# Performance work log

Hardware: AMD Instinct MI355X
Metric: run time of the kernel (lower is better)

The kernel has to match this reference:

```python
import jax, jax.numpy as jnp
import numpy as np

B, S, D_IN, D_OUT, H = 4, 2048, 1024, 1024, 16
HD = D_OUT // H  # 64


def setup_inputs() -> dict:
    key = jax.random.key(0)
    ks = jax.random.split(key, 6)
    s = 1.0 / np.sqrt(D_IN)
    return {
        "x": jax.random.normal(ks[0], (B, S, D_IN), dtype=jnp.float32),
        "Wq": jax.random.uniform(ks[1], (D_IN, D_OUT), jnp.float32, -s, s),
        "Wk": jax.random.uniform(ks[2], (D_IN, D_OUT), jnp.float32, -s, s),
        "Wv": jax.random.uniform(ks[3], (D_IN, D_OUT), jnp.float32, -s, s),
        "Wo": jax.random.uniform(ks[4], (D_OUT, D_OUT), jnp.float32, -s, s),
        "bo": jax.random.uniform(ks[5], (D_OUT,), jnp.float32, -s, s),
    }


def reference(x, Wq, Wk, Wv, Wo, bo):
    b, s, _ = x.shape
    # QKV projections -> [b, H, s, hd]
    def split_heads(t):
        return t.reshape(b, s, H, HD).transpose(0, 2, 1, 3)
    q = split_heads(x @ Wq)
    k = split_heads(x @ Wk)
    v = split_heads(x @ Wv)
    # attention scores [b, H, s, s]
    scores = jnp.einsum("bhqd,bhkd->bhqk", q, k)
    causal = jnp.triu(jnp.ones((s, s), dtype=bool), k=1)
    scores = jnp.where(causal, -jnp.inf, scores)
    attn = jax.nn.softmax(scores / np.sqrt(HD), axis=-1)
    ctx = jnp.einsum("bhqk,bhkd->bhqd", attn, v)
    ctx = ctx.transpose(0, 2, 1, 3).reshape(b, s, D_OUT)
    return ctx @ Wo + bo
```

## Files before the change

kernel.cpp:

```cpp
#include <hip/hip_runtime.h>

typedef __attribute__((ext_vector_type(8))) short bf16x8;
typedef __attribute__((ext_vector_type(4))) float f32x4;
typedef __attribute__((ext_vector_type(4))) unsigned uint4v;

#define SM_C 0.18033688011112042f
#define SM_M 20.0f
#define MFMA16 __builtin_amdgcn_mfma_f32_16x16x32_bf16

__device__ __forceinline__ unsigned short f2bf(float f) {
  unsigned u = __builtin_bit_cast(unsigned, f);
  u += 0x7fffu + ((u >> 16) & 1u);
  return (unsigned short)(u >> 16);
}

__device__ __forceinline__ unsigned cvtpk(float lo, float hi) {
  unsigned r;
  asm volatile("v_cvt_pk_bf16_f32 %0, %1, %2" : "=v"(r) : "v"(lo), "v"(hi));
  return r;
}

__device__ __forceinline__ void gload16(const void* g, void* lds) {
  __builtin_amdgcn_global_load_lds(
      (const __attribute__((address_space(1))) void*)g,
      (__attribute__((address_space(3))) void*)lds, 16, 0, 0);
}

#define BARRIER __builtin_amdgcn_s_barrier()
#define LGKM0 asm volatile("s_waitcnt lgkmcnt(0)" ::: "memory")

__global__ __launch_bounds__(256) void prep(const float* __restrict__ x,
                                            unsigned short* __restrict__ xb,
                                            const float* __restrict__ W0,
                                            const float* __restrict__ W1,
                                            const float* __restrict__ W2,
                                            const float* __restrict__ W3,
                                            unsigned short* __restrict__ WT) {
  __shared__ float tile[32][33];
  const int bid = blockIdx.x;
  if (bid < 2048) {
    int i = bid * 256 + threadIdx.x;
    for (; i < 2097152; i += 2048 * 256) {
      float4 v = ((const float4*)x)[i];
      unsigned long long packed = (unsigned long long)f2bf(v.x) |
                                  ((unsigned long long)f2bf(v.y) << 16) |
                                  ((unsigned long long)f2bf(v.z) << 32) |
                                  ((unsigned long long)f2bf(v.w) << 48);
      ((unsigned long long*)xb)[i] = packed;
    }
  } else {
    int b2 = bid - 2048;
    const int z = b2 >> 10;
    b2 &= 1023;
    const int bx = b2 & 31, by = b2 >> 5;
    const float* W = (z == 0) ? W0 : (z == 1) ? W1 : (z == 2) ? W2 : W3;
    unsigned short* WTo = WT + (size_t)z * 1048576;
    const int tx = threadIdx.x & 31, ty = threadIdx.x >> 5;
    const int xcol = bx * 32 + tx;
    for (int i = 0; i < 4; ++i) {
      int r = ty + i * 8;
      tile[r][tx] = W[(by * 32 + r) * 1024 + xcol];
    }
    __syncthreads();
    const int nx = by * 32 + tx;
    for (int i = 0; i < 4; ++i) {
      int r = ty + i * 8;
      WTo[(long)(bx * 32 + r) * 1024 + nx] = f2bf(tile[tx][r]);
    }
  }
}

template <int NR, int MODE>
__global__ __launch_bounds__(512, 1) void gemm3b(const unsigned short* __restrict__ A,
                                                 const unsigned short* __restrict__ BT,
                                                 unsigned short* __restrict__ Cb,
                                                 float* __restrict__ Cf,
                                                 const float* __restrict__ bias,
                                                 int M, int N, int K) {
  constexpr int BN = NR * 32;
  constexpr int NU = BN / 64;
  __shared__ alignas(16) unsigned short As[3][256 * 64];
  __shared__ alignas(16) unsigned short Bs[2][BN * 64];

  const int nbn = N / BN;
  const int tmg = (M / 256) / 8;
  const int cc = blockIdx.x >> 3, xc = blockIdx.x & 7;
  const int tm = xc * tmg + cc / nbn, tn = cc % nbn;

  const int t = threadIdx.x, l = t & 63, wid = t >> 6;
  const int wm = wid >> 1, wn = wid & 1;
  const int lr = l & 15, lg = l >> 4;

  f32x4 acc[4][NR] = {};

  const int sq = t >> 3;
  const int sslot8 = ((t & 7) ^ (sq & 7)) * 8;
  const unsigned short* Ath = A + ((long)tm * 256 + sq) * K + sslot8;
  const unsigned short* Bth = BT + ((long)tn * BN + sq) * K + sslot8;
  const int ldsoff = sq * 64 + (t & 7) * 8;

#define STGA(buf, q, kt) \
  gload16(Ath + (long)((q)*64) * K + (kt)*64, &As[buf][(q)*4096 + ldsoff])
#define STGB(buf, u, kt) \
  gload16(Bth + (long)((u)*64) * K + (kt)*64, &Bs[buf][(u)*4096 + ldsoff])

  const int NT = K >> 6;
#pragma unroll
  for (int q = 0; q < 4; ++q) STGA(0, q, 0);
#pragma unroll
  for (int u = 0; u < NU; ++u) STGB(0, u, 0);
#pragma unroll
  for (int q = 0; q < 4; ++q) STGA(1, q, 1);

  const int offk0 = (lg ^ (lr & 7)) * 8;
  const int offk1 = ((4 + lg) ^ (lr & 7)) * 8;
  const int arow0 = (wm * 64 + lr) * 64;
  const int brow0 = (wn * (NR * 16) + lr) * 64;

#define DS_A(MH)                                                   \
  _Pragma("unroll") for (int m_ = 0; m_ < 2; ++m_) {               \
    const unsigned short* ap_ = Ac + arow0 + ((MH)*2 + m_) * 1024; \
    af[m_][0] = *(const bf16x8*)(ap_ + offk0);                     \
    af[m_][1] = *(const bf16x8*)(ap_ + offk1);                     \
  }
#define DS_B_ALL                                          \
  _Pragma("unroll") for (int n_ = 0; n_ < NR; ++n_) {     \
    const unsigned short* bp_ = Bc + brow0 + n_ * 1024;   \
    bfr[n_][0] = *(const bf16x8*)(bp_ + offk0);           \
    bfr[n_][1] = *(const bf16x8*)(bp_ + offk1);           \
  }
#define MM(MH)                                                              \
  __builtin_amdgcn_s_setprio(1);                                            \
  _Pragma("unroll") for (int m_ = 0; m_ < 2; ++m_)                          \
  _Pragma("unroll") for (int n_ = 0; n_ < NR; ++n_) {                       \
    acc[(MH)*2 + m_][n_] = MFMA16(af[m_][0], bfr[n_][0],                    \
                                  acc[(MH)*2 + m_][n_], 0, 0, 0);           \
    acc[(MH)*2 + m_][n_] = MFMA16(af[m_][1], bfr[n_][1],                    \
                                  acc[(MH)*2 + m_][n_], 0, 0, 0);           \
  }                                                                         \
  __builtin_amdgcn_s_setprio(0);

  int cur3 = 0;
  int stg3 = 2;
  for (int tt = 0; tt < NT; ++tt) {
    const unsigned short* Ac = As[cur3];
    const unsigned short* Bc = Bs[tt & 1];

    bf16x8 af[2][2];
    bf16x8 bfr[NR][2];

    if (tt == NT - 1) asm volatile("s_waitcnt vmcnt(0)" ::: "memory");
    else              asm volatile("s_waitcnt vmcnt(4)" ::: "memory");
    BARRIER;
    DS_A(0);
    DS_B_ALL;
    if (tt + 1 < NT) {
      const int nbB = (tt + 1) & 1;
#pragma unroll
      for (int u = 0; u < NU; ++u) STGB(nbB, u, tt + 1);
    }
    BARRIER;
    LGKM0;
    MM(0);

    DS_A(1);
    if (tt + 2 < NT) {
#pragma unroll
      for (int q = 0; q < 4; ++q) STGA(stg3, q, tt + 2);
    }
    BARRIER;
    LGKM0;
    MM(1);

    cur3 = (cur3 == 2) ? 0 : cur3 + 1;
    stg3 = (stg3 == 2) ? 0 : stg3 + 1;
  }
#undef DS_A
#undef DS_B_ALL
#undef MM
#undef STGA
#undef STGB

  const long crow = (long)tm * 256 + wm * 64;
  const int ccol = tn * BN + wn * (NR * 16);

  if constexpr (MODE == 1) {
#pragma unroll
    for (int m = 0; m < 4; ++m)
#pragma unroll
      for (int n = 0; n < NR; ++n)
#pragma unroll
        for (int r = 0; r < 4; ++r) {
          long row = crow + m * 16 + lg * 4 + r;
          int col = ccol + n * 16 + lr;
          Cf[row * N + col] = acc[m][n][r] + bias[col];
        }
  } else {
#pragma unroll
    for (int n = 0; n < NR; ++n) {
      const int colg = ccol + n * 16;
      const int plane = colg >> 10;
      if (plane < 2) {
        unsigned short* pl = Cb + (size_t)plane * 8388608;
        const int pc = (colg & 1023) + lr;
#pragma unroll
        for (int m = 0; m < 4; ++m)
#pragma unroll
          for (int r = 0; r < 4; ++r) {
            long row = crow + m * 16 + lg * 4 + r;
            pl[row * 1024 + pc] = f2bf(acc[m][n][r]);
          }
      } else {
        unsigned short* VtW = Cb + 16777216;
        const int bq = (tm >> 3) << 4;
        const int sbase = ((tm & 7) << 8) + wm * 64;
        const int vcol = (colg & 1023) + lr;
        const long vtrow = (long)(bq + (vcol >> 6)) * 64 + (vcol & 63);
#pragma unroll
        for (int m = 0; m < 4; ++m) {
          const int srow_ = sbase + m * 16 + lg * 4;
          const int lwb = srow_ & 63;
          const int stt = srow_ >> 6;
          const int vp0 = (lwb & 32) | (((lwb >> 2) & 3) << 3) | (((lwb >> 4) & 1) << 2);
          unsigned long long pk4 =
              (unsigned long long)f2bf(acc[m][n][0]) |
              ((unsigned long long)f2bf(acc[m][n][1]) << 16) |
              ((unsigned long long)f2bf(acc[m][n][2]) << 32) |
              ((unsigned long long)f2bf(acc[m][n][3]) << 48);
          *(unsigned long long*)(VtW + vtrow * 2048 + stt * 64 + vp0) = pk4;
        }
      }
    }
  }
}

template <int TWO>
__device__ __forceinline__ void attn_tile(
    const unsigned short* __restrict__ Kc, const unsigned short* __restrict__ Vc,
    int lr, int lg, bool mask0, bool mask1, int kv0, int q0row, int q1row,
    const bf16x8 (&qf)[2][2], f32x4 (&cacc)[2][4], float (&l_r)[2]) {
  constexpr int S0 = TWO ? 0 : 1;
  f32x4 p[2][4];
#pragma unroll
  for (int s = S0; s < 2; ++s)
#pragma unroll
    for (int g = 0; g < 4; ++g) p[s][g] = f32x4{0.f, 0.f, 0.f, 0.f};

  __builtin_amdgcn_s_setprio(1);
#pragma unroll
  for (int g = 0; g < 4; ++g) {
    const int key = g * 16 + lr;
    const int swz = (key & 7) << 3;
#pragma unroll
    for (int c = 0; c < 2; ++c) {
      bf16x8 kf = *(const bf16x8*)(Kc + key * 64 + ((c * 32 + lg * 8) ^ swz));
#pragma unroll
      for (int s = S0; s < 2; ++s)
        p[s][g] = MFMA16(kf, qf[s][c], p[s][g], 0, 0, 0);
    }
  }
  __builtin_amdgcn_s_setprio(0);

  if (TWO && mask0) {
#pragma unroll
    for (int g = 0; g < 4; ++g)
#pragma unroll
      for (int r = 0; r < 4; ++r)
        if (kv0 + g * 16 + lg * 4 + r > q0row) p[0][g][r] = -1e30f;
  }
  if (mask1) {
#pragma unroll
    for (int g = 0; g < 4; ++g)
#pragma unroll
      for (int r = 0; r < 4; ++r)
        if (kv0 + g * 16 + lg * 4 + r > q1row) p[1][g][r] = -1e30f;
  }

  const float SM_NMC = -SM_M * SM_C;
  unsigned pk[2][4][2];
#pragma unroll
  for (int s = S0; s < 2; ++s) {
    float e[4][4];
#pragma unroll
    for (int g = 0; g < 4; ++g)
#pragma unroll
      for (int r = 0; r < 4; ++r)
        e[g][r] = __builtin_amdgcn_exp2f(__builtin_fmaf(p[s][g][r], SM_C, SM_NMC));
    float t0 = (e[0][0] + e[0][1]) + (e[0][2] + e[0][3]);
    float t1 = (e[1][0] + e[1][1]) + (e[1][2] + e[1][3]);
    float t2 = (e[2][0] + e[2][1]) + (e[2][2] + e[2][3]);
    float t3 = (e[3][0] + e[3][1]) + (e[3][2] + e[3][3]);
    l_r[s] += (t0 + t1) + (t2 + t3);
#pragma unroll
    for (int g = 0; g < 4; ++g) {
      pk[s][g][0] = cvtpk(e[g][0], e[g][1]);
      pk[s][g][1] = cvtpk(e[g][2], e[g][3]);
    }
  }

#pragma unroll
  for (int sl = 0; sl < 2; ++sl) {
    bf16x8 vf[4];
#pragma unroll
    for (int n = 0; n < 4; ++n) {
      const int hd = n * 16 + lr;
      vf[n] = *(const bf16x8*)(Vc + hd * 64 + ((sl * 32 + lg * 8) ^ ((hd & 7) << 3)));
    }
    __builtin_amdgcn_s_setprio(1);
#pragma unroll
    for (int s = S0; s < 2; ++s) {
      uint4v pw = {pk[s][2 * sl][0], pk[s][2 * sl][1], pk[s][2 * sl + 1][0], pk[s][2 * sl + 1][1]};
      bf16x8 pa = __builtin_bit_cast(bf16x8, pw);
#pragma unroll
      for (int n = 0; n < 4; ++n)
        cacc[s][n] = MFMA16(pa, vf[n], cacc[s][n], 0, 0, 0);
    }
    __builtin_amdgcn_s_setprio(0);
  }
}

__global__ __launch_bounds__(256, 4) void flash_attn(const unsigned short* __restrict__ Qp,
                                                     const unsigned short* __restrict__ Kp,
                                                     const unsigned short* __restrict__ Vt,
                                                     unsigned short* __restrict__ Ctx) {
  __shared__ alignas(16) unsigned short Ks[2][64 * 64];
  __shared__ alignas(16) unsigned short Vs[2][64 * 64];
  const int bid = blockIdx.x;
  const int xcd = bid & 7;
  const int rest = bid >> 3;
  const int bh = xcd * 8 + (rest & 7);
  const int qt = rest >> 3;
  const int b = bh >> 4, h = bh & 15;
  const int t = threadIdx.x, l = t & 63, w = t >> 6;
  const int lr = l & 15, lg = l >> 4;
  const long rowbase = (long)b * 2048;
  const int colbase = h * 64;
  const int q0 = qt * 64 + w * 16;
  const int q1 = (31 - qt) * 64 + w * 16;
  const int q0row = q0 + lr, q1row = q1 + lr;
  const int nkv = 32 - qt;

  bf16x8 qf[2][2];
#pragma unroll
  for (int c = 0; c < 2; ++c) {
    qf[0][c] = *(const bf16x8*)(Qp + (rowbase + q0 + lr) * 1024 + colbase + c * 32 + lg * 8);
    qf[1][c] = *(const bf16x8*)(Qp + (rowbase + q1 + lr) * 1024 + colbase + c * 32 + lg * 8);
  }

  f32x4 cacc[2][4];
  float l_r[2];
#pragma unroll
  for (int s = 0; s < 2; ++s) {
    l_r[s] = 0.f;
#pragma unroll
    for (int n = 0; n < 4; ++n) cacc[s][n] = f32x4{0.f, 0.f, 0.f, 0.f};
  }

  const int srow = w * 16 + (l >> 3);
  const int scol = (l & 7) * 8;
  const int kswz = scol ^ ((srow & 7) << 3);
  const unsigned short* kp = Kp + (rowbase + srow) * 1024 + colbase + kswz;
  const unsigned short* vp = Vt + ((long)(bh * 64 + srow)) * 2048 + kswz;
  unsigned short* ksd0 = &Ks[0][(w * 16) * 64];
  unsigned short* vsd0 = &Vs[0][(w * 16) * 64];

#define STAGE(buf)                                    \
  do {                                                \
    gload16(kp, ksd0 + (buf) * 4096);                 \
    gload16(kp + 8 * 1024, ksd0 + (buf) * 4096 + 512);\
    gload16(vp, vsd0 + (buf) * 4096);                 \
    gload16(vp + 8 * 2048, vsd0 + (buf) * 4096 + 512);\
    kp += 64 * 1024;                                  \
    vp += 64;                                         \
  } while (0)

#define TILE_WAIT(j)                                                          \
  do {                                                                        \
    if ((j) == nkv - 1) asm volatile("s_waitcnt vmcnt(0)" ::: "memory");      \
    else                asm volatile("s_waitcnt vmcnt(4)" ::: "memory");      \
    asm volatile("s_barrier" ::: "memory");                                   \
  } while (0)

  STAGE(0);
  STAGE(1);

  int j = 0;
  for (; j <= qt; ++j) {
    const int cur = j & 1;
    TILE_WAIT(j);
    attn_tile<1>(Ks[cur], Vs[cur], lr, lg, j == qt, false, j * 64, q0row, q1row,
                 qf, cacc, l_r);
    asm volatile("s_barrier" ::: "memory");
    if (j + 2 < nkv) STAGE(cur);
  }
  for (; j < nkv; ++j) {
    const int cur = j & 1;
    TILE_WAIT(j);
    attn_tile<0>(Ks[cur], Vs[cur], lr, lg, false, j == nkv - 1, j * 64, q0row, q1row,
                 qf, cacc, l_r);
    asm volatile("s_barrier" ::: "memory");
    if (j + 2 < nkv) STAGE(cur);
  }
#undef STAGE
#undef TILE_WAIT

#pragma unroll
  for (int s = 0; s < 2; ++s) {
    float rs = l_r[s];
    rs += __shfl_xor(rs, 16);
    rs += __shfl_xor(rs, 32);
    float invl = 1.f / rs;
    float ilq[4];
#pragma unroll
    for (int r = 0; r < 4; ++r) ilq[r] = __shfl(invl, lg * 20 + r);
    const int qs = (s == 0) ? q0 : q1;
#pragma unroll
    for (int n = 0; n < 4; ++n)
#pragma unroll
      for (int r = 0; r < 4; ++r) {
        long row = rowbase + qs + lg * 4 + r;
        Ctx[row * 1024 + colbase + n * 16 + lr] = f2bf(cacc[s][n][r] * ilq[r]);
      }
  }
}

extern "C" void kernel_launch(void* const* d_in, const int* in_sizes, int n_in,
                              void* d_out, int out_size, void* d_ws, size_t ws_size,
                              hipStream_t stream) {
  (void)in_sizes; (void)n_in; (void)out_size; (void)ws_size;
  const float* x  = (const float*)d_in[0];
  const float* Wq = (const float*)d_in[1];
  const float* Wk = (const float*)d_in[2];
  const float* Wv = (const float*)d_in[3];
  const float* Wo = (const float*)d_in[4];
  const float* bo = (const float*)d_in[5];
  float* out = (float*)d_out;

  unsigned short* ws = (unsigned short*)d_ws;
  unsigned short* xb  = ws;
  unsigned short* WqT = ws + 8388608;
  unsigned short* WoT = WqT + 3145728;
  unsigned short* QKV = WqT + 4194304;
  unsigned short* Qp  = QKV;
  unsigned short* Kp  = QKV + 8388608;
  unsigned short* Vt  = QKV + 16777216;
  unsigned short* Ctx = QKV + 25165824;

  prep<<<6144, 256, 0, stream>>>(x, xb, Wq, Wk, Wv, Wo, WqT);

  gemm3b<6, 0><<<512, 512, 0, stream>>>(xb, WqT, QKV, nullptr, nullptr,
                                        8192, 3072, 1024);

  flash_attn<<<1024, 256, 0, stream>>>(Qp, Kp, Vt, Ctx);

  gemm3b<4, 1><<<256, 512, 0, stream>>>(Ctx, WoT, nullptr, out, bo,
                                        8192, 1024, 1024);
}
```

Baseline: 135.9 us.

## Merge two query-tile pairs per flash-attention block to share K/V staging

The flash-attention kernel now runs 512-thread blocks made of two 4-wave groups. Group 0 handles the query tile pair (qt, 31-qt) and group 1 handles (qt+8, 23-qt), and both read one shared double-buffered K/V tile stream from LDS. Each thread now issues one global-to-LDS load per tensor per tile, and the grid is halved. This is meant to cut redundant K/V global traffic and staging work. The cost is that group 1 finishes its causal range eight tiles early and then just waits at barriers, so some waves sit idle and may hurt load balance.

Result: no change. 136.0 us (+0.1%).

```diff
diff --git a/kernel.cpp b/kernel.cpp
--- a/kernel.cpp
+++ b/kernel.cpp
@@ -319,7 +319,7 @@
   }
 }
 
-__global__ __launch_bounds__(256, 4) void flash_attn(const unsigned short* __restrict__ Qp,
+__global__ __launch_bounds__(512, 4) void flash_attn(const unsigned short* __restrict__ Qp,
                                                      const unsigned short* __restrict__ Kp,
                                                      const unsigned short* __restrict__ Vt,
                                                      unsigned short* __restrict__ Ctx) {
@@ -332,11 +332,14 @@
   const int qt = rest >> 3;
   const int b = bh >> 4, h = bh & 15;
   const int t = threadIdx.x, l = t & 63, w = t >> 6;
+  const int wq = w & 3, grp = w >> 2;
   const int lr = l & 15, lg = l >> 4;
   const long rowbase = (long)b * 2048;
   const int colbase = h * 64;
-  const int q0 = qt * 64 + w * 16;
-  const int q1 = (31 - qt) * 64 + w * 16;
+  const int p0 = qt + (grp << 3);
+  const int p1 = 31 - qt - (grp << 3);
+  const int q0 = p0 * 64 + wq * 16;
+  const int q1 = p1 * 64 + wq * 16;
   const int q0row = q0 + lr, q1row = q1 + lr;
   const int nkv = 32 - qt;
 
@@ -356,48 +359,42 @@
     for (int n = 0; n < 4; ++n) cacc[s][n] = f32x4{0.f, 0.f, 0.f, 0.f};
   }
 
-  const int srow = w * 16 + (l >> 3);
-  const int scol = (l & 7) * 8;
+  const int srow = t >> 3;
+  const int scol = (t & 7) * 8;
   const int kswz = scol ^ ((srow & 7) << 3);
   const unsigned short* kp = Kp + (rowbase + srow) * 1024 + colbase + kswz;
   const unsigned short* vp = Vt + ((long)(bh * 64 + srow)) * 2048 + kswz;
-  unsigned short* ksd0 = &Ks[0][(w * 16) * 64];
-  unsigned short* vsd0 = &Vs[0][(w * 16) * 64];
-
-#define STAGE(buf)                                    \
-  do {                                                \
-    gload16(kp, ksd0 + (buf) * 4096);                 \
-    gload16(kp + 8 * 1024, ksd0 + (buf) * 4096 + 512);\
-    gload16(vp, vsd0 + (buf) * 4096);                 \
-    gload16(vp + 8 * 2048, vsd0 + (buf) * 4096 + 512);\
-    kp += 64 * 1024;                                  \
-    vp += 64;                                         \
+  unsigned short* ksd0 = &Ks[0][w * 512];
+  unsigned short* vsd0 = &Vs[0][w * 512];
+
+#define STAGE(buf)                     \
+  do {                                 \
+    gload16(kp, ksd0 + (buf) * 4096);  \
+    gload16(vp, vsd0 + (buf) * 4096);  \
+    kp += 64 * 1024;                   \
+    vp += 64;                          \
   } while (0)
 
 #define TILE_WAIT(j)                                                          \
   do {                                                                        \
     if ((j) == nkv - 1) asm volatile("s_waitcnt vmcnt(0)" ::: "memory");      \
-    else                asm volatile("s_waitcnt vmcnt(4)" ::: "memory");      \
+    else                asm volatile("s_waitcnt vmcnt(2)" ::: "memory");      \
     asm volatile("s_barrier" ::: "memory");                                   \
   } while (0)
 
   STAGE(0);
   STAGE(1);
 
-  int j = 0;
-  for (; j <= qt; ++j) {
+  for (int j = 0; j < nkv; ++j) {
     const int cur = j & 1;
     TILE_WAIT(j);
-    attn_tile<1>(Ks[cur], Vs[cur], lr, lg, j == qt, false, j * 64, q0row, q1row,
-                 qf, cacc, l_r);
-    asm volatile("s_barrier" ::: "memory");
-    if (j + 2 < nkv) STAGE(cur);
-  }
-  for (; j < nkv; ++j) {
-    const int cur = j & 1;
-    TILE_WAIT(j);
-    attn_tile<0>(Ks[cur], Vs[cur], lr, lg, false, j == nkv - 1, j * 64, q0row, q1row,
-                 qf, cacc, l_r);
+    if (j <= p0) {
+      attn_tile<1>(Ks[cur], Vs[cur], lr, lg, j == p0, j == p1, j * 64,
+                   q0row, q1row, qf, cacc, l_r);
+    } else if (j <= p1) {
+      attn_tile<0>(Ks[cur], Vs[cur], lr, lg, false, j == p1, j * 64,
+                   q0row, q1row, qf, cacc, l_r);
+    }
     asm volatile("s_barrier" ::: "memory");
     if (j + 2 < nkv) STAGE(cur);
   }
@@ -451,7 +448,7 @@
   gemm3b<6, 0><<<512, 512, 0, stream>>>(xb, WqT, QKV, nullptr, nullptr,
                                         8192, 3072, 1024);
 
-  flash_attn<<<1024, 256, 0, stream>>>(Qp, Kp, Vt, Ctx);
+  flash_attn<<<512, 512, 0, stream>>>(Qp, Kp, Vt, Ctx);
 
   gemm3b<4, 1><<<256, 512, 0, stream>>>(Ctx, WoT, nullptr, out, bo,
                                         8192, 1024, 1024);
```
